# Kernel optimization log

Hardware: AMD Instinct MI355X
Metric: run time of the kernel (lower is better)

Reference implementation:

```python
import jax, jax.numpy as jnp
import numpy as np

N = 50000
E = 800000
IN_CH = 128
HID = 64
HEADS = 4
G = 64  # number of graphs in batch
NEG_SLOPE = 0.2


def setup_inputs() -> dict:
    key = jax.random.key(0)
    ks = jax.random.split(key, 16)
    s = lambda fan_in: 1.0 / np.sqrt(fan_in)
    x = jax.random.normal(ks[0], (N, IN_CH), dtype=jnp.float32)
    edge_index = jax.random.randint(ks[1], (2, E), 0, N, dtype=jnp.int64)
    batch = jnp.sort(jax.random.randint(ks[2], (N,), 0, G, dtype=jnp.int64))
    # GAT layer 1: in 128 -> heads*hid = 256
    W1 = jax.random.uniform(ks[3], (IN_CH, HEADS * HID), jnp.float32, -s(IN_CH), s(IN_CH))
    a1_src = jax.random.uniform(ks[4], (HEADS, HID), jnp.float32, -s(HID), s(HID))
    a1_dst = jax.random.uniform(ks[5], (HEADS, HID), jnp.float32, -s(HID), s(HID))
    b1 = jnp.zeros((HEADS * HID,), jnp.float32)
    # GAT layer 2: in 256 -> heads*hid = 256
    W2 = jax.random.uniform(ks[6], (HEADS * HID, HEADS * HID), jnp.float32, -s(HEADS * HID), s(HEADS * HID))
    a2_src = jax.random.uniform(ks[7], (HEADS, HID), jnp.float32, -s(HID), s(HID))
    a2_dst = jax.random.uniform(ks[8], (HEADS, HID), jnp.float32, -s(HID), s(HID))
    b2 = jnp.zeros((HEADS * HID,), jnp.float32)
    # post-pool MLP: (in + 2*heads*hid) -> 256 -> 128
    d_cat = IN_CH + 2 * HEADS * HID
    W3 = jax.random.uniform(ks[9], (d_cat, 256), jnp.float32, -s(d_cat), s(d_cat))
    b3 = jnp.zeros((256,), jnp.float32)
    W4 = jax.random.uniform(ks[10], (256, 128), jnp.float32, -s(256), s(256))
    b4 = jnp.zeros((128,), jnp.float32)
    return {"x": x, "edge_index": edge_index, "batch": batch,
            "W1": W1, "a1_src": a1_src, "a1_dst": a1_dst, "b1": b1,
            "W2": W2, "a2_src": a2_src, "a2_dst": a2_dst, "b2": b2,
            "W3": W3, "b3": b3, "W4": W4, "b4": b4}


def gat_layer(x, src, dst, W, a_src, a_dst, b):
    n = x.shape[0]
    h = (x @ W).reshape(n, HEADS, HID)                 # [N,H,D]
    e_src = jnp.einsum('nhd,hd->nh', h, a_src)         # [N,H]
    e_dst = jnp.einsum('nhd,hd->nh', h, a_dst)
    e = jax.nn.leaky_relu(e_src[src] + e_dst[dst], NEG_SLOPE)  # [E,H]
    # segment softmax over incoming edges of each destination node
    m = jax.ops.segment_max(e, dst, num_segments=n)
    m = jnp.where(jnp.isfinite(m), m, 0.0)
    ex = jnp.exp(e - m[dst])
    denom = jax.ops.segment_sum(ex, dst, num_segments=n)
    alpha = ex / (denom[dst] + 1e-16)                  # [E,H]
    msg = h[src] * alpha[:, :, None]                   # [E,H,D]
    out = jax.ops.segment_sum(msg, dst, num_segments=n)
    return out.reshape(n, HEADS * HID) + b


def reference(x, edge_index, batch, W1, a1_src, a1_dst, b1, W2, a2_src, a2_dst, b2, W3, b3, W4, b4):
    src, dst = edge_index[0], edge_index[1]
    h0 = x
    h1 = jax.nn.relu(gat_layer(h0, src, dst, W1, a1_src, a1_dst, b1))
    h2 = jax.nn.relu(gat_layer(h1, src, dst, W2, a2_src, a2_dst, b2))
    comb = jnp.concatenate([h0, h1, h2], axis=-1)      # [N, 128+256+256]
    sums = jax.ops.segment_sum(comb, batch, num_segments=G)
    cnt = jax.ops.segment_sum(jnp.ones((x.shape[0],), comb.dtype), batch, num_segments=G)
    pooled = sums / jnp.maximum(cnt, 1.0)[:, None]     # [G, 640]
    hmlp = jax.nn.relu(pooled @ W3 + b3)               # dropout is identity at eval
    return hmlp @ W4 + b4                              # [G, 128]
```

## Files before the change

kernel.cpp:

```cpp
#include <hip/hip_runtime.h>
#include <cstdint>
#include <cstddef>

#define N_NODES 50000
#define M_PAD 50048
#define E_EDGES 800000
#define INCH 128
#define HID 64
#define HEADS 4
#define NHD 256
#define NGRAPH 64
#define DCAT 640
#define NEG_SLOPE 0.2f

typedef __attribute__((ext_vector_type(8))) short bf16x8;
typedef __attribute__((ext_vector_type(4))) float f32x4;

static __device__ inline unsigned short f2bf(float f) {
    unsigned int u = __float_as_uint(f);
    unsigned int r = (u + 0x7FFFu + ((u >> 16) & 1u)) >> 16;
    return (unsigned short)r;
}
static __device__ inline float bf2f(unsigned short b) {
    return __uint_as_float(((unsigned int)b) << 16);
}

#define W1N (INCH * NHD)
#define W2N (NHD * NHD)
#define XN  (N_NODES * INCH)
#define HB  ((E_EDGES + 255) / 256)
#define GB  ((N_NODES + 255) / 256)
#define PZB ((NGRAPH * DCAT + 255) / 256)
#define SPB ((W1N + W2N + XN + 255) / 256)
#define PREPB (HB + GB + PZB + SPB)

__global__ void prep_kernel(
    const int* __restrict__ ei, const int* __restrict__ batch,
    const float* __restrict__ W1, const float* __restrict__ W2,
    const float* __restrict__ x,
    int* __restrict__ counts, int* __restrict__ goff,
    float* __restrict__ psums,
    unsigned short* __restrict__ w1thi, unsigned short* __restrict__ w1tlo,
    unsigned short* __restrict__ w2thi, unsigned short* __restrict__ w2tlo,
    unsigned short* __restrict__ xhi, unsigned short* __restrict__ xlo)
{
    const int b = blockIdx.x;
    if (b < HB) {
        const int e = b * 256 + threadIdx.x;
        if (e < E_EDGES) atomicAdd(&counts[ei[E_EDGES + e]], 1);
        return;
    }
    if (b < HB + GB) {
        const int n = (b - HB) * 256 + threadIdx.x;
        if (n >= N_NODES) return;
        const int bb = batch[n];
        const int bp = (n == 0) ? -1 : batch[n - 1];
        for (int g = bp + 1; g <= bb; ++g) goff[g] = n;
        if (n == N_NODES - 1)
            for (int g = bb + 1; g <= NGRAPH; ++g) goff[g] = N_NODES;
        return;
    }
    if (b < HB + GB + PZB) {
        const int i = (b - HB - GB) * 256 + threadIdx.x;
        if (i < NGRAPH * DCAT) psums[i] = 0.f;
        return;
    }
    const int i = (b - HB - GB - PZB) * 256 + threadIdx.x;
    float v; unsigned short* dhi; unsigned short* dlo; int idx;
    if (i < W1N) {
        const int n = i / INCH, k = i - n * INCH;
        v = W1[(size_t)k * NHD + n]; dhi = w1thi; dlo = w1tlo; idx = i;
    } else if (i < W1N + W2N) {
        const int j = i - W1N;
        const int n = j / NHD, k = j - n * NHD;
        v = W2[(size_t)k * NHD + n]; dhi = w2thi; dlo = w2tlo; idx = j;
    } else {
        const int j = i - W1N - W2N;
        if (j >= XN) return;
        v = x[j]; dhi = xhi; dlo = xlo; idx = j;
    }
    const unsigned short h = f2bf(v);
    dhi[idx] = h;
    dlo[idx] = f2bf(v - bf2f(h));
}

#define GK 32
#define LDA 40

__global__ __launch_bounds__(256, 2) void gemm_mfma(
    const unsigned short* __restrict__ Athi,
    const unsigned short* __restrict__ Atlo,
    const unsigned short* __restrict__ Bthi,
    const unsigned short* __restrict__ Btlo,
    const float* __restrict__ asrc, const float* __restrict__ adst,
    unsigned short* __restrict__ Cb, float* __restrict__ es,
    float* __restrict__ ed, int M, int K)
{
    __shared__ unsigned short Ahi[128 * LDA];
    __shared__ unsigned short Alo[128 * LDA];
    __shared__ unsigned short Bhi[256 * LDA];
    __shared__ unsigned short Blo[256 * LDA];

    const int t    = threadIdx.x;
    const int row0 = blockIdx.x * 128;
    const int wave = t >> 6, lane = t & 63;
    const int wr  = (wave >> 1) * 64;
    const int wc2 = (wave & 1) * 128;
    const int m16 = lane & 15, quad = lane >> 4;

    f32x4 acc[4][8];
#pragma unroll
    for (int i = 0; i < 4; ++i)
#pragma unroll
        for (int j = 0; j < 8; ++j) acc[i][j] = (f32x4){0.f, 0.f, 0.f, 0.f};

    for (int k0 = 0; k0 < K; k0 += GK) {
#pragma unroll
        for (int i = 0; i < 2; ++i) {
            const int seg = t + i * 256;
            const int r = seg >> 2, p = (seg & 3) * 8;
            const size_t ga = (size_t)(row0 + r) * K + k0 + p;
            *(int4*)(&Ahi[r * LDA + p]) = *(const int4*)(Athi + ga);
            *(int4*)(&Alo[r * LDA + p]) = *(const int4*)(Atlo + ga);
        }
#pragma unroll
        for (int i = 0; i < 4; ++i) {
            const int seg = t + i * 256;
            const int r = seg >> 2, p = (seg & 3) * 8;
            const size_t gb = (size_t)r * K + k0 + p;
            *(int4*)(&Bhi[r * LDA + p]) = *(const int4*)(Bthi + gb);
            *(int4*)(&Blo[r * LDA + p]) = *(const int4*)(Btlo + gb);
        }
        __syncthreads();

        bf16x8 afh[4], afl[4];
#pragma unroll
        for (int i = 0; i < 4; ++i) {
            const int r = wr + i * 16 + m16;
            afh[i] = *(const bf16x8*)(&Ahi[r * LDA + quad * 8]);
            afl[i] = *(const bf16x8*)(&Alo[r * LDA + quad * 8]);
        }
#pragma unroll
        for (int j = 0; j < 8; ++j) {
            const int n = wc2 + j * 16 + m16;
            const bf16x8 bh = *(const bf16x8*)(&Bhi[n * LDA + quad * 8]);
            const bf16x8 bl = *(const bf16x8*)(&Blo[n * LDA + quad * 8]);
#pragma unroll
            for (int i = 0; i < 4; ++i) {
                acc[i][j] = __builtin_amdgcn_mfma_f32_16x16x32_bf16(afh[i], bh, acc[i][j], 0, 0, 0);
                acc[i][j] = __builtin_amdgcn_mfma_f32_16x16x32_bf16(afh[i], bl, acc[i][j], 0, 0, 0);
                acc[i][j] = __builtin_amdgcn_mfma_f32_16x16x32_bf16(afl[i], bh, acc[i][j], 0, 0, 0);
            }
        }
        __syncthreads();
    }

#pragma unroll
    for (int i = 0; i < 4; ++i)
#pragma unroll
        for (int reg = 0; reg < 4; ++reg) {
            const int r = row0 + wr + i * 16 + quad * 4 + reg;
            if (r < M) {
#pragma unroll
                for (int j = 0; j < 8; ++j)
                    Cb[(size_t)r * NHD + wc2 + j * 16 + m16] = f2bf(acc[i][j][reg]);
            }
        }

    const int hbase = wc2 >> 6;
    float a_s0[4], a_d0[4], a_s1[4], a_d1[4];
#pragma unroll
    for (int j = 0; j < 4; ++j) {
        a_s0[j] = asrc[hbase * HID + j * 16 + m16];
        a_d0[j] = adst[hbase * HID + j * 16 + m16];
        a_s1[j] = asrc[(hbase + 1) * HID + j * 16 + m16];
        a_d1[j] = adst[(hbase + 1) * HID + j * 16 + m16];
    }
#pragma unroll
    for (int i = 0; i < 4; ++i)
#pragma unroll
        for (int reg = 0; reg < 4; ++reg) {
            float ps0 = 0.f, pd0 = 0.f, ps1 = 0.f, pd1 = 0.f;
#pragma unroll
            for (int j = 0; j < 4; ++j) {
                const float v0 = acc[i][j][reg];
                const float v1 = acc[i][j + 4][reg];
                ps0 += v0 * a_s0[j];
                pd0 += v0 * a_d0[j];
                ps1 += v1 * a_s1[j];
                pd1 += v1 * a_d1[j];
            }
#pragma unroll
            for (int off = 1; off < 16; off <<= 1) {
                ps0 += __shfl_xor(ps0, off, 64);
                pd0 += __shfl_xor(pd0, off, 64);
                ps1 += __shfl_xor(ps1, off, 64);
                pd1 += __shfl_xor(pd1, off, 64);
            }
            if (m16 == 0) {
                const int r = row0 + wr + i * 16 + quad * 4 + reg;
                if (r < M) {
                    es[r * HEADS + hbase]     = ps0;
                    ed[r * HEADS + hbase]     = pd0;
                    es[r * HEADS + hbase + 1] = ps1;
                    ed[r * HEADS + hbase + 1] = pd1;
                }
            }
        }
}

__global__ __launch_bounds__(256, 2) void gemm_mfma2(
    const unsigned short* __restrict__ At,
    const unsigned short* __restrict__ Bthi,
    const unsigned short* __restrict__ Btlo,
    const float* __restrict__ asrc, const float* __restrict__ adst,
    unsigned short* __restrict__ Cb, float* __restrict__ es,
    float* __restrict__ ed, int M, int K)
{
    __shared__ unsigned short Ash[128 * LDA];
    __shared__ unsigned short Bhi[256 * LDA];
    __shared__ unsigned short Blo[256 * LDA];

    const int t    = threadIdx.x;
    const int row0 = blockIdx.x * 128;
    const int wave = t >> 6, lane = t & 63;
    const int wr  = (wave >> 1) * 64;
    const int wc2 = (wave & 1) * 128;
    const int m16 = lane & 15, quad = lane >> 4;

    f32x4 acc[4][8];
#pragma unroll
    for (int i = 0; i < 4; ++i)
#pragma unroll
        for (int j = 0; j < 8; ++j) acc[i][j] = (f32x4){0.f, 0.f, 0.f, 0.f};

    for (int k0 = 0; k0 < K; k0 += GK) {
#pragma unroll
        for (int i = 0; i < 2; ++i) {
            const int seg = t + i * 256;
            const int r = seg >> 2, p = (seg & 3) * 8;
            *(int4*)(&Ash[r * LDA + p]) = *(const int4*)(At + (size_t)(row0 + r) * K + k0 + p);
        }
#pragma unroll
        for (int i = 0; i < 4; ++i) {
            const int seg = t + i * 256;
            const int r = seg >> 2, p = (seg & 3) * 8;
            const size_t gb = (size_t)r * K + k0 + p;
            *(int4*)(&Bhi[r * LDA + p]) = *(const int4*)(Bthi + gb);
            *(int4*)(&Blo[r * LDA + p]) = *(const int4*)(Btlo + gb);
        }
        __syncthreads();

        bf16x8 af[4];
#pragma unroll
        for (int i = 0; i < 4; ++i) {
            const int r = wr + i * 16 + m16;
            af[i] = *(const bf16x8*)(&Ash[r * LDA + quad * 8]);
        }
#pragma unroll
        for (int j = 0; j < 8; ++j) {
            const int n = wc2 + j * 16 + m16;
            const bf16x8 bh = *(const bf16x8*)(&Bhi[n * LDA + quad * 8]);
            const bf16x8 bl = *(const bf16x8*)(&Blo[n * LDA + quad * 8]);
#pragma unroll
            for (int i = 0; i < 4; ++i) {
                acc[i][j] = __builtin_amdgcn_mfma_f32_16x16x32_bf16(af[i], bh, acc[i][j], 0, 0, 0);
                acc[i][j] = __builtin_amdgcn_mfma_f32_16x16x32_bf16(af[i], bl, acc[i][j], 0, 0, 0);
            }
        }
        __syncthreads();
    }

#pragma unroll
    for (int i = 0; i < 4; ++i)
#pragma unroll
        for (int reg = 0; reg < 4; ++reg) {
            const int r = row0 + wr + i * 16 + quad * 4 + reg;
            if (r < M) {
#pragma unroll
                for (int j = 0; j < 8; ++j)
                    Cb[(size_t)r * NHD + wc2 + j * 16 + m16] = f2bf(acc[i][j][reg]);
            }
        }

    const int hbase = wc2 >> 6;
    float a_s0[4], a_d0[4], a_s1[4], a_d1[4];
#pragma unroll
    for (int j = 0; j < 4; ++j) {
        a_s0[j] = asrc[hbase * HID + j * 16 + m16];
        a_d0[j] = adst[hbase * HID + j * 16 + m16];
        a_s1[j] = asrc[(hbase + 1) * HID + j * 16 + m16];
        a_d1[j] = adst[(hbase + 1) * HID + j * 16 + m16];
    }
#pragma unroll
    for (int i = 0; i < 4; ++i)
#pragma unroll
        for (int reg = 0; reg < 4; ++reg) {
            float ps0 = 0.f, pd0 = 0.f, ps1 = 0.f, pd1 = 0.f;
#pragma unroll
            for (int j = 0; j < 4; ++j) {
                const float v0 = acc[i][j][reg];
                const float v1 = acc[i][j + 4][reg];
                ps0 += v0 * a_s0[j];
                pd0 += v0 * a_d0[j];
                ps1 += v1 * a_s1[j];
                pd1 += v1 * a_d1[j];
            }
#pragma unroll
            for (int off = 1; off < 16; off <<= 1) {
                ps0 += __shfl_xor(ps0, off, 64);
                pd0 += __shfl_xor(pd0, off, 64);
                ps1 += __shfl_xor(ps1, off, 64);
                pd1 += __shfl_xor(pd1, off, 64);
            }
            if (m16 == 0) {
                const int r = row0 + wr + i * 16 + quad * 4 + reg;
                if (r < M) {
                    es[r * HEADS + hbase]     = ps0;
                    ed[r * HEADS + hbase]     = pd0;
                    es[r * HEADS + hbase + 1] = ps1;
                    ed[r * HEADS + hbase + 1] = pd1;
                }
            }
        }
}

#define SBLK 1024
#define NSCB ((N_NODES + SBLK - 1) / SBLK)

__global__ __launch_bounds__(1024) void scan_local_kernel(
    const int* __restrict__ counts, int* __restrict__ offsets,
    int* __restrict__ bsum)
{
    __shared__ int tmp[SBLK];
    const int t = threadIdx.x;
    const int i = blockIdx.x * SBLK + t;
    const int v = (i < N_NODES) ? counts[i] : 0;
    tmp[t] = v;
    __syncthreads();
    for (int off = 1; off < SBLK; off <<= 1) {
        const int u = (t >= off) ? tmp[t - off] : 0;
        __syncthreads();
        tmp[t] += u;
        __syncthreads();
    }
    if (i < N_NODES) offsets[i] = tmp[t] - v;
    if (t == SBLK - 1) bsum[blockIdx.x] = tmp[t];
}

__global__ __launch_bounds__(1024) void scan_final_kernel(
    int* __restrict__ offsets, int* __restrict__ cursor,
    const int* __restrict__ bsum)
{
    __shared__ int base_sh;
    const int b = blockIdx.x;
    if (threadIdx.x == 0) {
        int s = 0;
        for (int j = 0; j < b; ++j) s += bsum[j];
        base_sh = s;
    }
    __syncthreads();
    const int i = b * SBLK + threadIdx.x;
    if (i < N_NODES) {
        const int v = offsets[i] + base_sh;
        offsets[i] = v;
        cursor[i]  = v;
    }
    if (b == 0 && threadIdx.x == 0) offsets[N_NODES] = E_EDGES;
}

__global__ void scatter_kernel(const int* __restrict__ ei, int* __restrict__ cursor,
                               int* __restrict__ csr)
{
    const int e = blockIdx.x * 256 + threadIdx.x;
    if (e >= E_EDGES) return;
    const int s = ei[e];
    const int d = ei[E_EDGES + e];
    const int pos = atomicAdd(&cursor[d], 1);
    csr[pos] = s;
}

__global__ __launch_bounds__(256) void aggregate_fused(
    const unsigned short* __restrict__ hb, const int* __restrict__ csr,
    const int* __restrict__ offsets,
    const float* __restrict__ es, const float* __restrict__ ed,
    const float* __restrict__ bias, unsigned short* __restrict__ outhi)
{
    const int wid  = threadIdx.x >> 6;
    const int lane = threadIdx.x & 63;
    const int node = blockIdx.x * 4 + wid;
    if (node >= N_NODES) return;
    const int head = lane >> 4;
    const int col  = lane * 4;
    const int sub  = lane & 15;

    const float edc = ed[node * 4 + head];
    const int beg = offsets[node], end = offsets[node + 1];

    float4 acc = make_float4(0.f, 0.f, 0.f, 0.f);
    float dsum = 0.f;

    int base = beg;
    int m_cur = min(16, end - base);
    int s_cur = 0; float w_cur = 0.f;
    if (base < end && sub < m_cur) {
        s_cur = csr[base + sub];
        float u = es[s_cur * 4 + head] + edc;
        u = u > 0.f ? u : NEG_SLOPE * u;
        w_cur = expf(u);
    }

    while (base < end) {
        const int base_n = base + 16;
        const int m_nxt = min(16, end - base_n);
        int s_nxt = 0; float w_nxt = 0.f;
        if (base_n < end && sub < m_nxt) {
            s_nxt = csr[base_n + sub];
            float u = es[s_nxt * 4 + head] + edc;
            u = u > 0.f ? u : NEG_SLOPE * u;
            w_nxt = expf(u);
        }
        if (m_cur == 16) {
#pragma unroll
            for (int i = 0; i < 16; ++i) {
                const int   s = (int)__builtin_amdgcn_readlane((unsigned)s_cur, i);
                const float w = __shfl(w_cur, (lane & 48) + i, 64);
                const ushort4 v = *(const ushort4*)(hb + (size_t)s * NHD + col);
                acc.x += w * bf2f(v.x);
                acc.y += w * bf2f(v.y);
                acc.z += w * bf2f(v.z);
                acc.w += w * bf2f(v.w);
                dsum += w;
            }
        } else {
            for (int i = 0; i < m_cur; ++i) {
                const int   s = __shfl(s_cur, i, 64);
                const float w = __shfl(w_cur, (lane & 48) + i, 64);
                const ushort4 v = *(const ushort4*)(hb + (size_t)s * NHD + col);
                acc.x += w * bf2f(v.x);
                acc.y += w * bf2f(v.y);
                acc.z += w * bf2f(v.z);
                acc.w += w * bf2f(v.w);
                dsum += w;
            }
        }
        s_cur = s_nxt; w_cur = w_nxt; m_cur = m_nxt; base = base_n;
    }

    const float inv = 1.0f / (dsum + 1e-16f);
    const float4 bb = *(const float4*)(bias + col);
    float4 o;
    o.x = fmaxf(acc.x * inv + bb.x, 0.f);
    o.y = fmaxf(acc.y * inv + bb.y, 0.f);
    o.z = fmaxf(acc.z * inv + bb.z, 0.f);
    o.w = fmaxf(acc.w * inv + bb.w, 0.f);
    ushort4 oh;
    oh.x = f2bf(o.x); oh.y = f2bf(o.y); oh.z = f2bf(o.z); oh.w = f2bf(o.w);
    *(ushort4*)(outhi + (size_t)node * NHD + col) = oh;
}

#define PRB 128

__global__ __launch_bounds__(640) void pool_sum_kernel(
    const unsigned short* __restrict__ xhi, const unsigned short* __restrict__ h1b,
    const unsigned short* __restrict__ h2b, const int* __restrict__ batch,
    float* __restrict__ sums)
{
    __shared__ int bsh[PRB];
    const int c  = threadIdx.x;
    const int r0 = blockIdx.x * PRB;
    const int r1 = min(N_NODES, r0 + PRB);
    const int nr = r1 - r0;
    if (c < nr) bsh[c] = batch[r0 + c];
    __syncthreads();

    const unsigned short* srcb; int ld, cc;
    if (c < INCH)            { srcb = xhi; ld = INCH; cc = c; }
    else if (c < INCH + NHD) { srcb = h1b; ld = NHD;  cc = c - INCH; }
    else                     { srcb = h2b; ld = NHD;  cc = c - INCH - NHD; }

    float sum = 0.f;
    int g = bsh[0];
    for (int i = 0; i < nr; ++i) {
        const int gb = bsh[i];
        if (gb != g) {
            atomicAdd(&sums[g * DCAT + c], sum);
            sum = 0.f;
            g = gb;
        }
        sum += bf2f(srcb[(size_t)(r0 + i) * ld + cc]);
    }
    atomicAdd(&sums[g * DCAT + c], sum);
}

__global__ __launch_bounds__(256) void mlp_kernel(
    const float* __restrict__ psums, const int* __restrict__ goff,
    const float* __restrict__ W3, const float* __restrict__ b3,
    const float* __restrict__ W4, const float* __restrict__ b4,
    float* __restrict__ out)
{
    const int g = blockIdx.x;
    __shared__ float p[DCAT];
    __shared__ float hm[256];
    const float inv = 1.0f / fmaxf((float)(goff[g + 1] - goff[g]), 1.0f);
    for (int i = threadIdx.x; i < DCAT; i += 256)
        p[i] = psums[(size_t)g * DCAT + i] * inv;
    __syncthreads();
    const int c = threadIdx.x;
    float s = b3[c];
    for (int k = 0; k < DCAT; ++k) s += p[k] * W3[(size_t)k * 256 + c];
    hm[c] = fmaxf(s, 0.f);
    __syncthreads();
    if (c < 128) {
        float o = b4[c];
        for (int k = 0; k < 256; ++k) o += hm[k] * W4[(size_t)k * 128 + c];
        out[(size_t)g * 128 + c] = o;
    }
}

extern "C" void kernel_launch(void* const* d_in, const int* in_sizes, int n_in,
                              void* d_out, int out_size, void* d_ws, size_t ws_size,
                              hipStream_t stream)
{
    const float* x     = (const float*)d_in[0];
    const int*   ei    = (const int*)d_in[1];
    const int*   batch = (const int*)d_in[2];
    const float* W1    = (const float*)d_in[3];
    const float* a1s   = (const float*)d_in[4];
    const float* a1d   = (const float*)d_in[5];
    const float* b1    = (const float*)d_in[6];
    const float* W2    = (const float*)d_in[7];
    const float* a2s   = (const float*)d_in[8];
    const float* a2d   = (const float*)d_in[9];
    const float* b2    = (const float*)d_in[10];
    const float* W3    = (const float*)d_in[11];
    const float* b3    = (const float*)d_in[12];
    const float* W4    = (const float*)d_in[13];
    const float* b4    = (const float*)d_in[14];
    float* out = (float*)d_out;

    size_t off = 0;
    auto carve = [&](size_t bytes) -> void* {
        void* p = (char*)d_ws + off;
        off = (off + bytes + 255) & ~(size_t)255;
        return p;
    };
    unsigned short* xhi   = (unsigned short*)carve((size_t)M_PAD * INCH * 2);
    unsigned short* xlo   = (unsigned short*)carve((size_t)M_PAD * INCH * 2);
    unsigned short* ghi   = (unsigned short*)carve((size_t)N_NODES * NHD * 2);
    unsigned short* h1hi  = (unsigned short*)carve((size_t)M_PAD * NHD * 2);
    unsigned short* h2hi  = (unsigned short*)carve((size_t)N_NODES * NHD * 2);
    float* es     = (float*)carve((size_t)N_NODES * HEADS * 4);
    float* ed     = (float*)carve((size_t)N_NODES * HEADS * 4);
    float* psums  = (float*)carve((size_t)NGRAPH * DCAT * 4);
    int*   counts  = (int*)carve((size_t)N_NODES * 4);
    int*   offsets = (int*)carve((size_t)(N_NODES + 1) * 4);
    int*   cursor  = (int*)carve((size_t)N_NODES * 4);
    int*   csr     = (int*)carve((size_t)E_EDGES * 4);
    int*   goff    = (int*)carve((size_t)(NGRAPH + 1) * 4);
    int*   bsum    = (int*)carve((size_t)NSCB * 4);
    unsigned short* w1thi = (unsigned short*)carve((size_t)NHD * INCH * 2);
    unsigned short* w1tlo = (unsigned short*)carve((size_t)NHD * INCH * 2);
    unsigned short* w2thi = (unsigned short*)carve((size_t)NHD * NHD * 2);
    unsigned short* w2tlo = (unsigned short*)carve((size_t)NHD * NHD * 2);

    const int egrid = (E_EDGES + 255) / 256;

    hipMemsetAsync(counts, 0, (size_t)N_NODES * 4, stream);
    prep_kernel<<<PREPB, 256, 0, stream>>>(ei, batch, W1, W2, x,
                                           counts, goff, psums,
                                           w1thi, w1tlo, w2thi, w2tlo, xhi, xlo);
    scan_local_kernel<<<NSCB, SBLK, 0, stream>>>(counts, offsets, bsum);
    scan_final_kernel<<<NSCB, SBLK, 0, stream>>>(offsets, cursor, bsum);
    scatter_kernel<<<egrid, 256, 0, stream>>>(ei, cursor, csr);

    const int ggrid = M_PAD / 128;

    gemm_mfma<<<ggrid, 256, 0, stream>>>(xhi, xlo, w1thi, w1tlo, a1s, a1d,
                                         ghi, es, ed, N_NODES, INCH);
    aggregate_fused<<<(N_NODES + 3) / 4, 256, 0, stream>>>(ghi, csr, offsets,
                                                           es, ed, b1, h1hi);
    gemm_mfma2<<<ggrid, 256, 0, stream>>>(h1hi, w2thi, w2tlo, a2s, a2d,
                                          ghi, es, ed, N_NODES, NHD);
    aggregate_fused<<<(N_NODES + 3) / 4, 256, 0, stream>>>(ghi, csr, offsets,
                                                           es, ed, b2, h2hi);

    pool_sum_kernel<<<(N_NODES + PRB - 1) / PRB, 640, 0, stream>>>(xhi, h1hi, h2hi, batch, psums);
    mlp_kernel<<<NGRAPH, 256, 0, stream>>>(psums, goff, W3, b3, W4, b4, out);
}
```

Before: 438.3 us.

## Aggregate before projecting: fold attention vectors into weights, reorder GAT layers

The attention logits are now computed from W·a vectors precomputed in the prep kernel, so dedicated es kernels only need a small per-node dot product. Each layer aggregates the low-dimensional inputs over the CSR first and then applies the weight matrix with bias and ReLU in a GEMM. For layer 1 this gathers 128-wide x per edge instead of 256-wide h, at the cost of a per-head 4x128 aggregated buffer and a per-head GEMM. The x lo-part split is dropped, which lowers precision for layer 1.

```diff
diff --git a/kernel.cpp b/kernel.cpp
--- a/kernel.cpp
+++ b/kernel.cpp
@@ -32,17 +32,21 @@
 #define GB  ((N_NODES + 255) / 256)
 #define PZB ((NGRAPH * DCAT + 255) / 256)
 #define SPB ((W1N + W2N + XN + 255) / 256)
-#define PREPB (HB + GB + PZB + SPB)
+#define WAB ((INCH * 8 + NHD * 8 + 255) / 256)
+#define PREPB (HB + GB + PZB + SPB + WAB)
 
 __global__ void prep_kernel(
     const int* __restrict__ ei, const int* __restrict__ batch,
     const float* __restrict__ W1, const float* __restrict__ W2,
     const float* __restrict__ x,
+    const float* __restrict__ a1s, const float* __restrict__ a1d,
+    const float* __restrict__ a2s, const float* __restrict__ a2d,
     int* __restrict__ counts, int* __restrict__ goff,
     float* __restrict__ psums,
     unsigned short* __restrict__ w1thi, unsigned short* __restrict__ w1tlo,
     unsigned short* __restrict__ w2thi, unsigned short* __restrict__ w2tlo,
-    unsigned short* __restrict__ xhi, unsigned short* __restrict__ xlo)
+    unsigned short* __restrict__ xb,
+    float* __restrict__ W1a, float* __restrict__ W2a)
 {
     const int b = blockIdx.x;
     if (b < HB) {
@@ -65,264 +69,94 @@
         if (i < NGRAPH * DCAT) psums[i] = 0.f;
         return;
     }
-    const int i = (b - HB - GB - PZB) * 256 + threadIdx.x;
-    float v; unsigned short* dhi; unsigned short* dlo; int idx;
-    if (i < W1N) {
-        const int n = i / INCH, k = i - n * INCH;
-        v = W1[(size_t)k * NHD + n]; dhi = w1thi; dlo = w1tlo; idx = i;
-    } else if (i < W1N + W2N) {
-        const int j = i - W1N;
-        const int n = j / NHD, k = j - n * NHD;
-        v = W2[(size_t)k * NHD + n]; dhi = w2thi; dlo = w2tlo; idx = j;
-    } else {
-        const int j = i - W1N - W2N;
-        if (j >= XN) return;
-        v = x[j]; dhi = xhi; dlo = xlo; idx = j;
-    }
-    const unsigned short h = f2bf(v);
-    dhi[idx] = h;
-    dlo[idx] = f2bf(v - bf2f(h));
-}
-
-#define GK 32
-#define LDA 40
-
-__global__ __launch_bounds__(256, 2) void gemm_mfma(
-    const unsigned short* __restrict__ Athi,
-    const unsigned short* __restrict__ Atlo,
-    const unsigned short* __restrict__ Bthi,
-    const unsigned short* __restrict__ Btlo,
-    const float* __restrict__ asrc, const float* __restrict__ adst,
-    unsigned short* __restrict__ Cb, float* __restrict__ es,
-    float* __restrict__ ed, int M, int K)
-{
-    __shared__ unsigned short Ahi[128 * LDA];
-    __shared__ unsigned short Alo[128 * LDA];
-    __shared__ unsigned short Bhi[256 * LDA];
-    __shared__ unsigned short Blo[256 * LDA];
-
-    const int t    = threadIdx.x;
-    const int row0 = blockIdx.x * 128;
-    const int wave = t >> 6, lane = t & 63;
-    const int wr  = (wave >> 1) * 64;
-    const int wc2 = (wave & 1) * 128;
-    const int m16 = lane & 15, quad = lane >> 4;
-
-    f32x4 acc[4][8];
-#pragma unroll
-    for (int i = 0; i < 4; ++i)
-#pragma unroll
-        for (int j = 0; j < 8; ++j) acc[i][j] = (f32x4){0.f, 0.f, 0.f, 0.f};
-
-    for (int k0 = 0; k0 < K; k0 += GK) {
-#pragma unroll
-        for (int i = 0; i < 2; ++i) {
-            const int seg = t + i * 256;
-            const int r = seg >> 2, p = (seg & 3) * 8;
-            const size_t ga = (size_t)(row0 + r) * K + k0 + p;
-            *(int4*)(&Ahi[r * LDA + p]) = *(const int4*)(Athi + ga);
-            *(int4*)(&Alo[r * LDA + p]) = *(const int4*)(Atlo + ga);
-        }
-#pragma unroll
-        for (int i = 0; i < 4; ++i) {
-            const int seg = t + i * 256;
-            const int r = seg >> 2, p = (seg & 3) * 8;
-            const size_t gb = (size_t)r * K + k0 + p;
-            *(int4*)(&Bhi[r * LDA + p]) = *(const int4*)(Bthi + gb);
-            *(int4*)(&Blo[r * LDA + p]) = *(const int4*)(Btlo + gb);
-        }
-        __syncthreads();
-
-        bf16x8 afh[4], afl[4];
-#pragma unroll
-        for (int i = 0; i < 4; ++i) {
-            const int r = wr + i * 16 + m16;
-            afh[i] = *(const bf16x8*)(&Ahi[r * LDA + quad * 8]);
-            afl[i] = *(const bf16x8*)(&Alo[r * LDA + quad * 8]);
-        }
-#pragma unroll
-        for (int j = 0; j < 8; ++j) {
-            const int n = wc2 + j * 16 + m16;
-            const bf16x8 bh = *(const bf16x8*)(&Bhi[n * LDA + quad * 8]);
-            const bf16x8 bl = *(const bf16x8*)(&Blo[n * LDA + quad * 8]);
-#pragma unroll
-            for (int i = 0; i < 4; ++i) {
-                acc[i][j] = __builtin_amdgcn_mfma_f32_16x16x32_bf16(afh[i], bh, acc[i][j], 0, 0, 0);
-                acc[i][j] = __builtin_amdgcn_mfma_f32_16x16x32_bf16(afh[i], bl, acc[i][j], 0, 0, 0);
-                acc[i][j] = __builtin_amdgcn_mfma_f32_16x16x32_bf16(afl[i], bh, acc[i][j], 0, 0, 0);
-            }
-        }
-        __syncthreads();
-    }
-
-#pragma unroll
-    for (int i = 0; i < 4; ++i)
-#pragma unroll
-        for (int reg = 0; reg < 4; ++reg) {
-            const int r = row0 + wr + i * 16 + quad * 4 + reg;
-            if (r < M) {
-#pragma unroll
-                for (int j = 0; j < 8; ++j)
-                    Cb[(size_t)r * NHD + wc2 + j * 16 + m16] = f2bf(acc[i][j][reg]);
-            }
-        }
-
-    const int hbase = wc2 >> 6;
-    float a_s0[4], a_d0[4], a_s1[4], a_d1[4];
-#pragma unroll
-    for (int j = 0; j < 4; ++j) {
-        a_s0[j] = asrc[hbase * HID + j * 16 + m16];
-        a_d0[j] = adst[hbase * HID + j * 16 + m16];
-        a_s1[j] = asrc[(hbase + 1) * HID + j * 16 + m16];
-        a_d1[j] = adst[(hbase + 1) * HID + j * 16 + m16];
-    }
-#pragma unroll
-    for (int i = 0; i < 4; ++i)
-#pragma unroll
-        for (int reg = 0; reg < 4; ++reg) {
-            float ps0 = 0.f, pd0 = 0.f, ps1 = 0.f, pd1 = 0.f;
-#pragma unroll
-            for (int j = 0; j < 4; ++j) {
-                const float v0 = acc[i][j][reg];
-                const float v1 = acc[i][j + 4][reg];
-                ps0 += v0 * a_s0[j];
-                pd0 += v0 * a_d0[j];
-                ps1 += v1 * a_s1[j];
-                pd1 += v1 * a_d1[j];
-            }
-#pragma unroll
-            for (int off = 1; off < 16; off <<= 1) {
-                ps0 += __shfl_xor(ps0, off, 64);
-                pd0 += __shfl_xor(pd0, off, 64);
-                ps1 += __shfl_xor(ps1, off, 64);
-                pd1 += __shfl_xor(pd1, off, 64);
-            }
-            if (m16 == 0) {
-                const int r = row0 + wr + i * 16 + quad * 4 + reg;
-                if (r < M) {
-                    es[r * HEADS + hbase]     = ps0;
-                    ed[r * HEADS + hbase]     = pd0;
-                    es[r * HEADS + hbase + 1] = ps1;
-                    ed[r * HEADS + hbase + 1] = pd1;
-                }
-            }
-        }
-}
-
-__global__ __launch_bounds__(256, 2) void gemm_mfma2(
-    const unsigned short* __restrict__ At,
-    const unsigned short* __restrict__ Bthi,
-    const unsigned short* __restrict__ Btlo,
-    const float* __restrict__ asrc, const float* __restrict__ adst,
-    unsigned short* __restrict__ Cb, float* __restrict__ es,
-    float* __restrict__ ed, int M, int K)
-{
-    __shared__ unsigned short Ash[128 * LDA];
-    __shared__ unsigned short Bhi[256 * LDA];
-    __shared__ unsigned short Blo[256 * LDA];
-
-    const int t    = threadIdx.x;
-    const int row0 = blockIdx.x * 128;
-    const int wave = t >> 6, lane = t & 63;
-    const int wr  = (wave >> 1) * 64;
-    const int wc2 = (wave & 1) * 128;
-    const int m16 = lane & 15, quad = lane >> 4;
-
-    f32x4 acc[4][8];
-#pragma unroll
-    for (int i = 0; i < 4; ++i)
-#pragma unroll
-        for (int j = 0; j < 8; ++j) acc[i][j] = (f32x4){0.f, 0.f, 0.f, 0.f};
-
-    for (int k0 = 0; k0 < K; k0 += GK) {
-#pragma unroll
-        for (int i = 0; i < 2; ++i) {
-            const int seg = t + i * 256;
-            const int r = seg >> 2, p = (seg & 3) * 8;
-            *(int4*)(&Ash[r * LDA + p]) = *(const int4*)(At + (size_t)(row0 + r) * K + k0 + p);
-        }
-#pragma unroll
-        for (int i = 0; i < 4; ++i) {
-            const int seg = t + i * 256;
-            const int r = seg >> 2, p = (seg & 3) * 8;
-            const size_t gb = (size_t)r * K + k0 + p;
-            *(int4*)(&Bhi[r * LDA + p]) = *(const int4*)(Bthi + gb);
-            *(int4*)(&Blo[r * LDA + p]) = *(const int4*)(Btlo + gb);
-        }
-        __syncthreads();
-
-        bf16x8 af[4];
-#pragma unroll
-        for (int i = 0; i < 4; ++i) {
-            const int r = wr + i * 16 + m16;
-            af[i] = *(const bf16x8*)(&Ash[r * LDA + quad * 8]);
-        }
-#pragma unroll
-        for (int j = 0; j < 8; ++j) {
-            const int n = wc2 + j * 16 + m16;
-            const bf16x8 bh = *(const bf16x8*)(&Bhi[n * LDA + quad * 8]);
-            const bf16x8 bl = *(const bf16x8*)(&Blo[n * LDA + quad * 8]);
-#pragma unroll
-            for (int i = 0; i < 4; ++i) {
-                acc[i][j] = __builtin_amdgcn_mfma_f32_16x16x32_bf16(af[i], bh, acc[i][j], 0, 0, 0);
-                acc[i][j] = __builtin_amdgcn_mfma_f32_16x16x32_bf16(af[i], bl, acc[i][j], 0, 0, 0);
-            }
-        }
-        __syncthreads();
-    }
-
-#pragma unroll
-    for (int i = 0; i < 4; ++i)
-#pragma unroll
-        for (int reg = 0; reg < 4; ++reg) {
-            const int r = row0 + wr + i * 16 + quad * 4 + reg;
-            if (r < M) {
-#pragma unroll
-                for (int j = 0; j < 8; ++j)
-                    Cb[(size_t)r * NHD + wc2 + j * 16 + m16] = f2bf(acc[i][j][reg]);
-            }
-        }
-
-    const int hbase = wc2 >> 6;
-    float a_s0[4], a_d0[4], a_s1[4], a_d1[4];
-#pragma unroll
-    for (int j = 0; j < 4; ++j) {
-        a_s0[j] = asrc[hbase * HID + j * 16 + m16];
-        a_d0[j] = adst[hbase * HID + j * 16 + m16];
-        a_s1[j] = asrc[(hbase + 1) * HID + j * 16 + m16];
-        a_d1[j] = adst[(hbase + 1) * HID + j * 16 + m16];
-    }
-#pragma unroll
-    for (int i = 0; i < 4; ++i)
-#pragma unroll
-        for (int reg = 0; reg < 4; ++reg) {
-            float ps0 = 0.f, pd0 = 0.f, ps1 = 0.f, pd1 = 0.f;
-#pragma unroll
-            for (int j = 0; j < 4; ++j) {
-                const float v0 = acc[i][j][reg];
-                const float v1 = acc[i][j + 4][reg];
-                ps0 += v0 * a_s0[j];
-                pd0 += v0 * a_d0[j];
-                ps1 += v1 * a_s1[j];
-                pd1 += v1 * a_d1[j];
-            }
-#pragma unroll
-            for (int off = 1; off < 16; off <<= 1) {
-                ps0 += __shfl_xor(ps0, off, 64);
-                pd0 += __shfl_xor(pd0, off, 64);
-                ps1 += __shfl_xor(ps1, off, 64);
-                pd1 += __shfl_xor(pd1, off, 64);
-            }
-            if (m16 == 0) {
-                const int r = row0 + wr + i * 16 + quad * 4 + reg;
-                if (r < M) {
-                    es[r * HEADS + hbase]     = ps0;
-                    ed[r * HEADS + hbase]     = pd0;
-                    es[r * HEADS + hbase + 1] = ps1;
-                    ed[r * HEADS + hbase + 1] = pd1;
-                }
-            }
-        }
+    if (b < HB + GB + PZB + SPB) {
+        const int i = (b - HB - GB - PZB) * 256 + threadIdx.x;
+        if (i < W1N) {
+            const int n = i / INCH, k = i - n * INCH;
+            const float v = W1[(size_t)k * NHD + n];
+            const unsigned short h = f2bf(v);
+            w1thi[i] = h; w1tlo[i] = f2bf(v - bf2f(h));
+        } else if (i < W1N + W2N) {
+            const int j = i - W1N;
+            const int n = j / NHD, k = j - n * NHD;
+            const float v = W2[(size_t)k * NHD + n];
+            const unsigned short h = f2bf(v);
+            w2thi[j] = h; w2tlo[j] = f2bf(v - bf2f(h));
+        } else {
+            const int j = i - W1N - W2N;
+            if (j < XN) xb[j] = f2bf(x[j]);
+        }
+        return;
+    }
+    const int i = (b - HB - GB - PZB - SPB) * 256 + threadIdx.x;
+    if (i < INCH * 8) {
+        const int k = i >> 3, j = i & 7, h = j & 3;
+        const float* a = (j < 4) ? a1s : a1d;
+        float s = 0.f;
+        for (int d = 0; d < HID; ++d)
+            s += W1[(size_t)k * NHD + h * HID + d] * a[h * HID + d];
+        W1a[i] = s;
+    } else if (i < INCH * 8 + NHD * 8) {
+        const int i2 = i - INCH * 8;
+        const int k = i2 >> 3, j = i2 & 7, h = j & 3;
+        const float* a = (j < 4) ? a2s : a2d;
+        float s = 0.f;
+        for (int d = 0; d < HID; ++d)
+            s += W2[(size_t)k * NHD + h * HID + d] * a[h * HID + d];
+        W2a[i2] = s;
+    }
+}
+
+__global__ __launch_bounds__(256) void es1_kernel(
+    const float* __restrict__ x, const float* __restrict__ W1a,
+    float* __restrict__ es, float* __restrict__ ed)
+{
+    const int wid = threadIdx.x >> 6, lane = threadIdx.x & 63;
+    float wa[2][8];
+#pragma unroll
+    for (int r = 0; r < 2; ++r)
+#pragma unroll
+        for (int j = 0; j < 8; j += 4)
+            *(float4*)&wa[r][j] = *(const float4*)(W1a + (size_t)(lane * 2 + r) * 8 + j);
+    for (int node = blockIdx.x * 4 + wid; node < N_NODES; node += gridDim.x * 4) {
+        const float2 xv = *(const float2*)(x + (size_t)node * INCH + lane * 2);
+        float p[8];
+#pragma unroll
+        for (int j = 0; j < 8; ++j) p[j] = xv.x * wa[0][j] + xv.y * wa[1][j];
+#pragma unroll
+        for (int off = 1; off < 64; off <<= 1)
+#pragma unroll
+            for (int j = 0; j < 8; ++j) p[j] += __shfl_xor(p[j], off, 64);
+        if (lane < 4)       es[node * 4 + lane]     = p[lane];
+        else if (lane < 8)  ed[node * 4 + lane - 4] = p[lane];
+    }
+}
+
+__global__ __launch_bounds__(256) void es2_kernel(
+    const unsigned short* __restrict__ h1b, const float* __restrict__ W2a,
+    float* __restrict__ es, float* __restrict__ ed)
+{
+    const int wid = threadIdx.x >> 6, lane = threadIdx.x & 63;
+    float wa[4][8];
+#pragma unroll
+    for (int r = 0; r < 4; ++r)
+#pragma unroll
+        for (int j = 0; j < 8; j += 4)
+            *(float4*)&wa[r][j] = *(const float4*)(W2a + (size_t)(lane * 4 + r) * 8 + j);
+    for (int node = blockIdx.x * 4 + wid; node < N_NODES; node += gridDim.x * 4) {
+        const ushort4 hv = *(const ushort4*)(h1b + (size_t)node * NHD + lane * 4);
+        const float h0 = bf2f(hv.x), h1 = bf2f(hv.y), h2 = bf2f(hv.z), h3 = bf2f(hv.w);
+        float p[8];
+#pragma unroll
+        for (int j = 0; j < 8; ++j)
+            p[j] = h0 * wa[0][j] + h1 * wa[1][j] + h2 * wa[2][j] + h3 * wa[3][j];
+#pragma unroll
+        for (int off = 1; off < 64; off <<= 1)
+#pragma unroll
+            for (int j = 0; j < 8; ++j) p[j] += __shfl_xor(p[j], off, 64);
+        if (lane < 4)       es[node * 4 + lane]     = p[lane];
+        else if (lane < 8)  ed[node * 4 + lane - 4] = p[lane];
+    }
 }
 
 #define SBLK 1024
@@ -380,11 +214,181 @@
     csr[pos] = s;
 }
 
-__global__ __launch_bounds__(256) void aggregate_fused(
+__global__ __launch_bounds__(256) void aggregate1_kernel(
+    const unsigned short* __restrict__ xb, const int* __restrict__ csr,
+    const int* __restrict__ offsets,
+    const float* __restrict__ es, const float* __restrict__ ed,
+    unsigned short* __restrict__ xab)
+{
+    const int wid  = threadIdx.x >> 6;
+    const int lane = threadIdx.x & 63;
+    const int node = blockIdx.x * 4 + wid;
+    if (node >= N_NODES) return;
+    const int col = lane * 2;
+    const int sub = lane & 15;
+
+    const float4 edv = *(const float4*)(ed + node * 4);
+    const int beg = offsets[node], end = offsets[node + 1];
+
+    float acc[4][2] = {};
+    float ds[4] = {0.f, 0.f, 0.f, 0.f};
+
+    int base = beg;
+    int m_cur = min(16, end - base);
+    int s_cur = 0; float4 w_cur = make_float4(0.f, 0.f, 0.f, 0.f);
+    if (base < end && sub < m_cur) {
+        s_cur = csr[base + sub];
+        const float4 e4 = *(const float4*)(es + s_cur * 4);
+        float u0 = e4.x + edv.x, u1 = e4.y + edv.y;
+        float u2 = e4.z + edv.z, u3 = e4.w + edv.w;
+        u0 = u0 > 0.f ? u0 : NEG_SLOPE * u0;
+        u1 = u1 > 0.f ? u1 : NEG_SLOPE * u1;
+        u2 = u2 > 0.f ? u2 : NEG_SLOPE * u2;
+        u3 = u3 > 0.f ? u3 : NEG_SLOPE * u3;
+        w_cur = make_float4(expf(u0), expf(u1), expf(u2), expf(u3));
+    }
+
+    while (base < end) {
+        const int base_n = base + 16;
+        const int m_nxt = min(16, end - base_n);
+        int s_nxt = 0; float4 w_nxt = make_float4(0.f, 0.f, 0.f, 0.f);
+        if (base_n < end && sub < m_nxt) {
+            s_nxt = csr[base_n + sub];
+            const float4 e4 = *(const float4*)(es + s_nxt * 4);
+            float u0 = e4.x + edv.x, u1 = e4.y + edv.y;
+            float u2 = e4.z + edv.z, u3 = e4.w + edv.w;
+            u0 = u0 > 0.f ? u0 : NEG_SLOPE * u0;
+            u1 = u1 > 0.f ? u1 : NEG_SLOPE * u1;
+            u2 = u2 > 0.f ? u2 : NEG_SLOPE * u2;
+            u3 = u3 > 0.f ? u3 : NEG_SLOPE * u3;
+            w_nxt = make_float4(expf(u0), expf(u1), expf(u2), expf(u3));
+        }
+        if (m_cur == 16) {
+#pragma unroll
+            for (int i = 0; i < 16; ++i) {
+                const int   s  = (int)__builtin_amdgcn_readlane((unsigned)s_cur, i);
+                const float wx = __shfl(w_cur.x, i, 64);
+                const float wy = __shfl(w_cur.y, i, 64);
+                const float wz = __shfl(w_cur.z, i, 64);
+                const float ww = __shfl(w_cur.w, i, 64);
+                const unsigned int xv = *(const unsigned int*)(xb + (size_t)s * INCH + col);
+                const float x0 = bf2f((unsigned short)(xv & 0xFFFF));
+                const float x1 = bf2f((unsigned short)(xv >> 16));
+                acc[0][0] += wx * x0; acc[0][1] += wx * x1;
+                acc[1][0] += wy * x0; acc[1][1] += wy * x1;
+                acc[2][0] += wz * x0; acc[2][1] += wz * x1;
+                acc[3][0] += ww * x0; acc[3][1] += ww * x1;
+                ds[0] += wx; ds[1] += wy; ds[2] += wz; ds[3] += ww;
+            }
+        } else {
+            for (int i = 0; i < m_cur; ++i) {
+                const int   s  = __shfl(s_cur, i, 64);
+                const float wx = __shfl(w_cur.x, i, 64);
+                const float wy = __shfl(w_cur.y, i, 64);
+                const float wz = __shfl(w_cur.z, i, 64);
+                const float ww = __shfl(w_cur.w, i, 64);
+                const unsigned int xv = *(const unsigned int*)(xb + (size_t)s * INCH + col);
+                const float x0 = bf2f((unsigned short)(xv & 0xFFFF));
+                const float x1 = bf2f((unsigned short)(xv >> 16));
+                acc[0][0] += wx * x0; acc[0][1] += wx * x1;
+                acc[1][0] += wy * x0; acc[1][1] += wy * x1;
+                acc[2][0] += wz * x0; acc[2][1] += wz * x1;
+                acc[3][0] += ww * x0; acc[3][1] += ww * x1;
+                ds[0] += wx; ds[1] += wy; ds[2] += wz; ds[3] += ww;
+            }
+        }
+        s_cur = s_nxt; w_cur = w_nxt; m_cur = m_nxt; base = base_n;
+    }
+
+#pragma unroll
+    for (int h = 0; h < 4; ++h) {
+        const float inv = 1.0f / (ds[h] + 1e-16f);
+        unsigned int o = (unsigned int)f2bf(acc[h][0] * inv)
+                       | ((unsigned int)f2bf(acc[h][1] * inv) << 16);
+        *(unsigned int*)(xab + ((size_t)node * 4 + h) * INCH + col) = o;
+    }
+}
+
+#define GK 32
+#define LDA 40
+
+__global__ __launch_bounds__(256) void gemm_h1_kernel(
+    const unsigned short* __restrict__ xab,
+    const unsigned short* __restrict__ Bthi,
+    const unsigned short* __restrict__ Btlo,
+    const float* __restrict__ b1,
+    unsigned short* __restrict__ h1b, int M)
+{
+    __shared__ unsigned short Ash[128 * LDA];
+    __shared__ unsigned short Bh[64 * LDA];
+    __shared__ unsigned short Bl[64 * LDA];
+
+    const int head = blockIdx.y;
+    const int row0 = blockIdx.x * 128;
+    const int t = threadIdx.x, wave = t >> 6, lane = t & 63;
+    const int m16 = lane & 15, quad = lane >> 4;
+    const int wr = wave * 32;
+
+    f32x4 acc[2][4];
+#pragma unroll
+    for (int i = 0; i < 2; ++i)
+#pragma unroll
+        for (int j = 0; j < 4; ++j) acc[i][j] = (f32x4){0.f, 0.f, 0.f, 0.f};
+
+    for (int k0 = 0; k0 < INCH; k0 += GK) {
+#pragma unroll
+        for (int i = 0; i < 2; ++i) {
+            const int seg = t + i * 256;
+            const int r = seg >> 2, p = (seg & 3) * 8;
+            *(int4*)(&Ash[r * LDA + p]) =
+                *(const int4*)(xab + ((size_t)(row0 + r) * 4 + head) * INCH + k0 + p);
+        }
+        {
+            const int r = t >> 2, p = (t & 3) * 8;
+            const size_t gb = (size_t)(head * 64 + r) * INCH + k0 + p;
+            *(int4*)(&Bh[r * LDA + p]) = *(const int4*)(Bthi + gb);
+            *(int4*)(&Bl[r * LDA + p]) = *(const int4*)(Btlo + gb);
+        }
+        __syncthreads();
+
+        bf16x8 af[2];
+#pragma unroll
+        for (int i = 0; i < 2; ++i)
+            af[i] = *(const bf16x8*)(&Ash[(wr + i * 16 + m16) * LDA + quad * 8]);
+#pragma unroll
+        for (int j = 0; j < 4; ++j) {
+            const int n = j * 16 + m16;
+            const bf16x8 bh = *(const bf16x8*)(&Bh[n * LDA + quad * 8]);
+            const bf16x8 bl = *(const bf16x8*)(&Bl[n * LDA + quad * 8]);
+#pragma unroll
+            for (int i = 0; i < 2; ++i) {
+                acc[i][j] = __builtin_amdgcn_mfma_f32_16x16x32_bf16(af[i], bh, acc[i][j], 0, 0, 0);
+                acc[i][j] = __builtin_amdgcn_mfma_f32_16x16x32_bf16(af[i], bl, acc[i][j], 0, 0, 0);
+            }
+        }
+        __syncthreads();
+    }
+
+#pragma unroll
+    for (int i = 0; i < 2; ++i)
+#pragma unroll
+        for (int reg = 0; reg < 4; ++reg) {
+            const int r = row0 + wr + i * 16 + quad * 4 + reg;
+            if (r < M) {
+#pragma unroll
+                for (int j = 0; j < 4; ++j) {
+                    const int c = head * 64 + j * 16 + m16;
+                    h1b[(size_t)r * NHD + c] = f2bf(fmaxf(acc[i][j][reg] + b1[c], 0.f));
+                }
+            }
+        }
+}
+
+__global__ __launch_bounds__(256) void aggregate2_kernel(
     const unsigned short* __restrict__ hb, const int* __restrict__ csr,
     const int* __restrict__ offsets,
     const float* __restrict__ es, const float* __restrict__ ed,
-    const float* __restrict__ bias, unsigned short* __restrict__ outhi)
+    unsigned short* __restrict__ outb)
 {
     const int wid  = threadIdx.x >> 6;
     const int lane = threadIdx.x & 63;
@@ -448,21 +452,90 @@
     }
 
     const float inv = 1.0f / (dsum + 1e-16f);
-    const float4 bb = *(const float4*)(bias + col);
-    float4 o;
-    o.x = fmaxf(acc.x * inv + bb.x, 0.f);
-    o.y = fmaxf(acc.y * inv + bb.y, 0.f);
-    o.z = fmaxf(acc.z * inv + bb.z, 0.f);
-    o.w = fmaxf(acc.w * inv + bb.w, 0.f);
     ushort4 oh;
-    oh.x = f2bf(o.x); oh.y = f2bf(o.y); oh.z = f2bf(o.z); oh.w = f2bf(o.w);
-    *(ushort4*)(outhi + (size_t)node * NHD + col) = oh;
+    oh.x = f2bf(acc.x * inv); oh.y = f2bf(acc.y * inv);
+    oh.z = f2bf(acc.z * inv); oh.w = f2bf(acc.w * inv);
+    *(ushort4*)(outb + (size_t)node * NHD + col) = oh;
+}
+
+__global__ __launch_bounds__(256, 2) void gemm_h2_kernel(
+    const unsigned short* __restrict__ At,
+    const unsigned short* __restrict__ Bthi,
+    const unsigned short* __restrict__ Btlo,
+    const float* __restrict__ b2,
+    unsigned short* __restrict__ h2b, int M)
+{
+    __shared__ unsigned short Ash[128 * LDA];
+    __shared__ unsigned short Bhi[256 * LDA];
+    __shared__ unsigned short Blo[256 * LDA];
+
+    const int t    = threadIdx.x;
+    const int row0 = blockIdx.x * 128;
+    const int wave = t >> 6, lane = t & 63;
+    const int wr  = (wave >> 1) * 64;
+    const int wc2 = (wave & 1) * 128;
+    const int m16 = lane & 15, quad = lane >> 4;
+
+    f32x4 acc[4][8];
+#pragma unroll
+    for (int i = 0; i < 4; ++i)
+#pragma unroll
+        for (int j = 0; j < 8; ++j) acc[i][j] = (f32x4){0.f, 0.f, 0.f, 0.f};
+
+    for (int k0 = 0; k0 < NHD; k0 += GK) {
+#pragma unroll
+        for (int i = 0; i < 2; ++i) {
+            const int seg = t + i * 256;
+            const int r = seg >> 2, p = (seg & 3) * 8;
+            *(int4*)(&Ash[r * LDA + p]) = *(const int4*)(At + (size_t)(row0 + r) * NHD + k0 + p);
+        }
+#pragma unroll
+        for (int i = 0; i < 4; ++i) {
+            const int seg = t + i * 256;
+            const int r = seg >> 2, p = (seg & 3) * 8;
+            const size_t gb = (size_t)r * NHD + k0 + p;
+            *(int4*)(&Bhi[r * LDA + p]) = *(const int4*)(Bthi + gb);
+            *(int4*)(&Blo[r * LDA + p]) = *(const int4*)(Btlo + gb);
+        }
+        __syncthreads();
+
+        bf16x8 af[4];
+#pragma unroll
+        for (int i = 0; i < 4; ++i)
+            af[i] = *(const bf16x8*)(&Ash[(wr + i * 16 + m16) * LDA + quad * 8]);
+#pragma unroll
+        for (int j = 0; j < 8; ++j) {
+            const int n = wc2 + j * 16 + m16;
+            const bf16x8 bh = *(const bf16x8*)(&Bhi[n * LDA + quad * 8]);
+            const bf16x8 bl = *(const bf16x8*)(&Blo[n * LDA + quad * 8]);
+#pragma unroll
+            for (int i = 0; i < 4; ++i) {
+                acc[i][j] = __builtin_amdgcn_mfma_f32_16x16x32_bf16(af[i], bh, acc[i][j], 0, 0, 0);
+                acc[i][j] = __builtin_amdgcn_mfma_f32_16x16x32_bf16(af[i], bl, acc[i][j], 0, 0, 0);
+            }
+        }
+        __syncthreads();
+    }
+
+#pragma unroll
+    for (int i = 0; i < 4; ++i)
+#pragma unroll
+        for (int reg = 0; reg < 4; ++reg) {
+            const int r = row0 + wr + i * 16 + quad * 4 + reg;
+            if (r < M) {
+#pragma unroll
+                for (int j = 0; j < 8; ++j) {
+                    const int c = wc2 + j * 16 + m16;
+                    h2b[(size_t)r * NHD + c] = f2bf(fmaxf(acc[i][j][reg] + b2[c], 0.f));
+                }
+            }
+        }
 }
 
 #define PRB 128
 
 __global__ __launch_bounds__(640) void pool_sum_kernel(
-    const unsigned short* __restrict__ xhi, const unsigned short* __restrict__ h1b,
+    const unsigned short* __restrict__ xb, const unsigned short* __restrict__ h1b,
     const unsigned short* __restrict__ h2b, const int* __restrict__ batch,
     float* __restrict__ sums)
 {
@@ -475,7 +548,7 @@
     __syncthreads();
 
     const unsigned short* srcb; int ld, cc;
-    if (c < INCH)            { srcb = xhi; ld = INCH; cc = c; }
+    if (c < INCH)            { srcb = xb;  ld = INCH; cc = c; }
     else if (c < INCH + NHD) { srcb = h1b; ld = NHD;  cc = c - INCH; }
     else                     { srcb = h2b; ld = NHD;  cc = c - INCH - NHD; }
 
@@ -545,14 +618,16 @@
         off = (off + bytes + 255) & ~(size_t)255;
         return p;
     };
-    unsigned short* xhi   = (unsigned short*)carve((size_t)M_PAD * INCH * 2);
-    unsigned short* xlo   = (unsigned short*)carve((size_t)M_PAD * INCH * 2);
-    unsigned short* ghi   = (unsigned short*)carve((size_t)N_NODES * NHD * 2);
-    unsigned short* h1hi  = (unsigned short*)carve((size_t)M_PAD * NHD * 2);
-    unsigned short* h2hi  = (unsigned short*)carve((size_t)N_NODES * NHD * 2);
+    unsigned short* xb    = (unsigned short*)carve((size_t)M_PAD * INCH * 2);
+    unsigned short* xab   = (unsigned short*)carve((size_t)M_PAD * 4 * INCH * 2);
+    unsigned short* h1b   = (unsigned short*)carve((size_t)M_PAD * NHD * 2);
+    unsigned short* h1ab  = (unsigned short*)carve((size_t)M_PAD * NHD * 2);
+    unsigned short* h2b   = (unsigned short*)carve((size_t)N_NODES * NHD * 2);
     float* es     = (float*)carve((size_t)N_NODES * HEADS * 4);
     float* ed     = (float*)carve((size_t)N_NODES * HEADS * 4);
     float* psums  = (float*)carve((size_t)NGRAPH * DCAT * 4);
+    float* W1a    = (float*)carve((size_t)INCH * 8 * 4);
+    float* W2a    = (float*)carve((size_t)NHD * 8 * 4);
     int*   counts  = (int*)carve((size_t)N_NODES * 4);
     int*   offsets = (int*)carve((size_t)(N_NODES + 1) * 4);
     int*   cursor  = (int*)carve((size_t)N_NODES * 4);
@@ -568,23 +643,25 @@
 
     hipMemsetAsync(counts, 0, (size_t)N_NODES * 4, stream);
     prep_kernel<<<PREPB, 256, 0, stream>>>(ei, batch, W1, W2, x,
+                                           a1s, a1d, a2s, a2d,
                                            counts, goff, psums,
-                                           w1thi, w1tlo, w2thi, w2tlo, xhi, xlo);
+                                           w1thi, w1tlo, w2thi, w2tlo, xb,
+                                           W1a, W2a);
     scan_local_kernel<<<NSCB, SBLK, 0, stream>>>(counts, offsets, bsum);
     scan_final_kernel<<<NSCB, SBLK, 0, stream>>>(offsets, cursor, bsum);
     scatter_kernel<<<egrid, 256, 0, stream>>>(ei, cursor, csr);
 
-    const int ggrid = M_PAD / 128;
-
-    gemm_mfma<<<ggrid, 256, 0, stream>>>(xhi, xlo, w1thi, w1tlo, a1s, a1d,
-                                         ghi, es, ed, N_NODES, INCH);
-    aggregate_fused<<<(N_NODES + 3) / 4, 256, 0, stream>>>(ghi, csr, offsets,
-                                                           es, ed, b1, h1hi);
-    gemm_mfma2<<<ggrid, 256, 0, stream>>>(h1hi, w2thi, w2tlo, a2s, a2d,
-                                          ghi, es, ed, N_NODES, NHD);
-    aggregate_fused<<<(N_NODES + 3) / 4, 256, 0, stream>>>(ghi, csr, offsets,
-                                                           es, ed, b2, h2hi);
-
-    pool_sum_kernel<<<(N_NODES + PRB - 1) / PRB, 640, 0, stream>>>(xhi, h1hi, h2hi, batch, psums);
+    const int ngrid4 = (N_NODES + 3) / 4;
+
+    es1_kernel<<<391, 256, 0, stream>>>(x, W1a, es, ed);
+    aggregate1_kernel<<<ngrid4, 256, 0, stream>>>(xb, csr, offsets, es, ed, xab);
+    dim3 g1grid(M_PAD / 128, HEADS);
+    gemm_h1_kernel<<<g1grid, 256, 0, stream>>>(xab, w1thi, w1tlo, b1, h1b, N_NODES);
+
+    es2_kernel<<<391, 256, 0, stream>>>(h1b, W2a, es, ed);
+    aggregate2_kernel<<<ngrid4, 256, 0, stream>>>(h1b, csr, offsets, es, ed, h1ab);
+    gemm_h2_kernel<<<M_PAD / 128, 256, 0, stream>>>(h1ab, w2thi, w2tlo, b2, h2b, N_NODES);
+
+    pool_sum_kernel<<<(N_NODES + PRB - 1) / PRB, 640, 0, stream>>>(xb, h1b, h2b, batch, psums);
     mlp_kernel<<<NGRAPH, 256, 0, stream>>>(psums, goff, W3, b3, W4, b4, out);
 }
```

Measured after the change: 535.2 us. +22.1%, slower.
